# Optimization experiments

Measured on AMD Instinct MI355X. Metric: run time of the kernel, lower is better.

## Reference

```python
import jax, jax.numpy as jnp
import numpy as np

E = 16      # num_experts
K = 4       # num_experts_per_tok
H = 2048    # hidden_size
I = 1408    # moe_intermediate_size
SI = 5632   # shared expert intermediate size
CAP = 1024
NORM_TOPK = False


def setup_inputs() -> dict:
    key = jax.random.key(0)
    ks = jax.random.split(key, 9)
    def w(k, shape, fan_in):
        return jax.random.normal(k, shape, jnp.float32) * (fan_in ** -0.5)
    return {
        "hidden_states": jax.random.normal(ks[0], (1, 2048, H), jnp.float32),
        "gate_w":  w(ks[1], (E, H), H),        # router: Linear(H -> E), no bias
        "we_gate": w(ks[2], (E, I, H), H),     # per-expert gate_proj weights
        "we_up":   w(ks[3], (E, I, H), H),     # per-expert up_proj weights
        "we_down": w(ks[4], (E, H, I), I),     # per-expert down_proj weights
        "ws_gate": w(ks[5], (SI, H), H),       # shared expert gate_proj
        "ws_up":   w(ks[6], (SI, H), H),       # shared expert up_proj
        "ws_down": w(ks[7], (H, SI), SI),      # shared expert down_proj
        "sg_w":    w(ks[8], (1, H), H),        # shared_expert_gate: Linear(H -> 1)
    }


def reference(hidden_states, gate_w, we_gate, we_up, we_down,
              ws_gate, ws_up, ws_down, sg_w):
    B, S, Hd = hidden_states.shape
    x = hidden_states.reshape(-1, Hd)                      # [T, H]
    T = x.shape[0]

    # --- router ---
    router_logits = x @ gate_w.T                           # [T, E]
    probs = jax.nn.softmax(router_logits.astype(jnp.float32), axis=-1)
    topw, topi = jax.lax.top_k(probs, K)                   # [T, K]
    if NORM_TOPK:
        topw = topw / topw.sum(axis=-1, keepdims=True)

    # --- dispatch: flatten (token, slot) assignments ---
    A = T * K
    fe = topi.reshape(A)                                   # expert id per assignment
    fw = topw.reshape(A)                                   # routing weight per assignment
    ft = jnp.repeat(jnp.arange(T), K)                      # token id per assignment
    # position of each assignment within its expert (rank in arrival order)
    oh = jax.nn.one_hot(fe, E, dtype=jnp.int32)            # [A, E]
    pos = jnp.take_along_axis(jnp.cumsum(oh, axis=0) - 1, fe[:, None], axis=1)[:, 0]
    valid = pos < CAP
    # scatter tokens into per-expert buffers; overflow goes to dummy row CAP
    buf = jnp.zeros((E, CAP + 1, Hd), x.dtype)
    buf = buf.at[fe, jnp.where(valid, pos, CAP)].set(x[ft])[:, :CAP]  # [E, C, H]

    # --- per-expert SiLU-gated MLP (batched grouped GEMMs) ---
    g = jnp.einsum('ech,eih->eci', buf, we_gate)
    u = jnp.einsum('ech,eih->eci', buf, we_up)
    eo = jnp.einsum('eci,ehi->ech', jax.nn.silu(g) * u, we_down)      # [E, C, H]

    # --- combine: weighted scatter-add back to tokens ---
    ga = eo[fe, jnp.minimum(pos, CAP - 1)]                 # [A, H]
    wcomb = (fw * valid.astype(fw.dtype)).astype(x.dtype)
    y = jnp.zeros((T, Hd), x.dtype).at[ft].add(ga * wcomb[:, None])

    # --- shared expert with sigmoid gate ---
    sh = (jax.nn.silu(x @ ws_gate.T) * (x @ ws_up.T)) @ ws_down.T
    sh = jax.nn.sigmoid(x @ sg_w.T) * sh

    out = (y + sh).reshape(B, S, Hd)
    return out, router_logits
```

## Files before the change

### kernel.cpp

```cpp
#include <hip/hip_runtime.h>

#define T_TOK 2048
#define NE 16
#define KTOP 4
#define HD 2048
#define ID 1408
#define SID 5632
#define CAPACITY 1024

typedef __attribute__((ext_vector_type(8))) short short8;
typedef __attribute__((ext_vector_type(4))) float floatx4;

__device__ __forceinline__ short f2b(float f){
  union { float f; unsigned u; } v; v.f = f;
  unsigned r = v.u + 0x7fffu + ((v.u >> 16) & 1u);
  return (short)(r >> 16);
}
__device__ __forceinline__ float b2f(short s){
  union { float f; unsigned u; } v; v.u = ((unsigned)(unsigned short)s) << 16;
  return v.f;
}
__device__ __forceinline__ unsigned cvt_pk(float a, float b){
  unsigned r;
  asm("v_cvt_pk_bf16_f32 %0, %1, %2" : "=v"(r) : "v"(a), "v"(b));
  return r;
}
__device__ __forceinline__ short8 cvt8(float4 a, float4 b){
  union { unsigned d[4]; short8 s; } u;
  u.d[0] = cvt_pk(a.x, a.y); u.d[1] = cvt_pk(a.z, a.w);
  u.d[2] = cvt_pk(b.x, b.y); u.d[3] = cvt_pk(b.z, b.w);
  return u.s;
}
__device__ __forceinline__ void gl16(const void* g, void* l){
  __builtin_amdgcn_global_load_lds(
      (const __attribute__((address_space(1))) void*)g,
      (__attribute__((address_space(3))) void*)l, 16, 0, 0);
}

__global__ void moe_zero(int* __restrict__ counts){
  if (threadIdx.x < NE) counts[threadIdx.x] = 0;
}

__global__ void moe_convert(const float* __restrict__ eg, const float* __restrict__ eu,
                            const float* __restrict__ ed, const float* __restrict__ sgp,
                            const float* __restrict__ sup, const float* __restrict__ sdp,
                            short* __restrict__ dst)
{
  const long long R8 = 1441792LL;
  const int r = blockIdx.y;
  const float* src;
  if      (r <  4) src = eg  + (long long)r       * R8 * 8;
  else if (r <  8) src = eu  + (long long)(r - 4) * R8 * 8;
  else if (r < 12) src = ed  + (long long)(r - 8) * R8 * 8;
  else if (r == 12) src = sgp;
  else if (r == 13) src = sup;
  else              src = sdp;
  short8* d = (short8*)dst + (long long)r * R8;
  const long long stride = (long long)gridDim.x * blockDim.x;
  for (long long i = (long long)blockIdx.x * blockDim.x + threadIdx.x; i < R8; i += stride){
    float4 f0 = ((const float4*)src)[i * 2];
    float4 f1 = ((const float4*)src)[i * 2 + 1];
    d[i] = cvt8(f0, f1);
  }
}

__global__ void moe_router(const float* __restrict__ x,
                           const float* __restrict__ gate_w,
                           const float* __restrict__ sg_w,
                           float* __restrict__ logits_out,
                           short* __restrict__ xb,
                           int* __restrict__ counts,
                           int* __restrict__ slot_token,
                           float* __restrict__ slot_w,
                           int* __restrict__ tslot,
                           float* __restrict__ tw,
                           float* __restrict__ sg)
{
  int wave = threadIdx.x >> 6, lane = threadIdx.x & 63;
  int t = (blockIdx.x << 2) + wave;
  if (t >= T_TOK) return;
  const float4* xr = (const float4*)(x + (size_t)t * HD);
  short8* xbw = (short8*)(xb + (size_t)t * HD);
  float acc[17];
  #pragma unroll
  for (int e = 0; e < 17; ++e) acc[e] = 0.f;
  #pragma unroll
  for (int j = 0; j < 4; ++j){
    int i4 = (j * 64 + lane) * 2;
    float4 x0 = xr[i4], x1 = xr[i4 + 1];
    xbw[j * 64 + lane] = cvt8(x0, x1);
    #pragma unroll
    for (int e = 0; e < 16; ++e){
      const float4* gr = (const float4*)(gate_w + e * HD);
      float4 g0 = gr[i4], g1 = gr[i4 + 1];
      acc[e] += x0.x*g0.x + x0.y*g0.y + x0.z*g0.z + x0.w*g0.w
              + x1.x*g1.x + x1.y*g1.y + x1.z*g1.z + x1.w*g1.w;
    }
    const float4* sr = (const float4*)sg_w;
    float4 s0 = sr[i4], s1 = sr[i4 + 1];
    acc[16] += x0.x*s0.x + x0.y*s0.y + x0.z*s0.z + x0.w*s0.w
             + x1.x*s1.x + x1.y*s1.y + x1.z*s1.z + x1.w*s1.w;
  }
  #pragma unroll
  for (int e = 0; e < 17; ++e){
    float v = acc[e];
    #pragma unroll
    for (int off = 32; off > 0; off >>= 1) v += __shfl_xor(v, off, 64);
    acc[e] = v;
  }
  if (lane == 0){
    float m = acc[0];
    #pragma unroll
    for (int e = 1; e < 16; ++e) m = fmaxf(m, acc[e]);
    float p[16]; float s = 0.f;
    #pragma unroll
    for (int e = 0; e < 16; ++e){ p[e] = expf(acc[e] - m); s += p[e]; }
    float inv = 1.f / s;
    #pragma unroll
    for (int e = 0; e < 16; ++e) logits_out[t * 16 + e] = acc[e];
    unsigned used = 0;
    for (int k = 0; k < KTOP; ++k){
      float best = -1.f; int bi = 0;
      #pragma unroll
      for (int e = 0; e < 16; ++e){
        float pe = ((used >> e) & 1u) ? -1.f : p[e];
        if (pe > best){ best = pe; bi = e; }
      }
      used |= (1u << bi);
      int pos = atomicAdd(&counts[bi], 1);
      int enc = -1;
      if (pos < CAPACITY){
        slot_token[bi * CAPACITY + pos] = t;
        slot_w[bi * CAPACITY + pos] = best * inv;
        enc = bi * CAPACITY + pos;
      }
      tslot[t * KTOP + k] = enc;
      tw[t * KTOP + k] = best * inv;
    }
    sg[t] = 1.f / (1.f + expf(-acc[16]));
  }
}


#define GEMM_PREAMBLE \
  const int tid = threadIdx.x; \
  const int lane = tid & 63, wave = tid >> 6; \
  const int wr = wave >> 1, wc = wave & 1; \
  const int lrow = lane & 15, lk = lane >> 4; \
  const int s_th = (tid & 7) ^ ((tid >> 3) & 7); \
  const int koff = (s_th & 3) << 3; \
  const int rloc = ((tid >> 3) << 1) + (s_th >> 2); \
  const int lb = lrow >> 1; \
  const int soff = (((((lrow & 1) << 2) | lk) ^ (lb & 7)) << 4); \
  const int abase = (wr * 32 + lb) * 128 + soff;

__global__ __launch_bounds__(256) void moe_gateup(
    const short* __restrict__ Asrc,
    const short* __restrict__ Wg, const short* __restrict__ Wu,
    short* __restrict__ Out,
    const int* __restrict__ counts, const int* __restrict__ slot_token,
    int Ndim, int Kdim, int expert_mode, int mtiles, int ntiles)
{
  int nwg = gridDim.x;
  int wg = ((blockIdx.x & 7) * (nwg >> 3)) + (blockIdx.x >> 3);
  int m_t = wg % mtiles; wg /= mtiles;
  int n_t = wg % ntiles; int e = wg / ntiles;

  int cnt = T_TOK; size_t woff = 0; short* out = Out;
  if (expert_mode){
    cnt = counts[e]; if (cnt > CAPACITY) cnt = CAPACITY;
    if (m_t * 128 >= cnt) return;
    woff = (size_t)e * Ndim * Kdim;
    out = Out + (size_t)e * CAPACITY * Ndim;
  }
  const int m0 = m_t * 128, n0 = n_t * 64;

  __shared__ __align__(16) char smem[2][16384];

  GEMM_PREAMBLE
  const int gbase = 8192 + (wc * 16 + lb) * 128 + soff;

  const short* aP[2];
  #pragma unroll
  for (int i = 0; i < 2; ++i){
    int p = m0 + i * 64 + rloc;
    const short* base;
    if (expert_mode){
      int q = (p < cnt) ? p : 0;
      base = Asrc + (size_t)slot_token[e * CAPACITY + q] * Kdim;
    } else base = Asrc + (size_t)p * Kdim;
    aP[i] = base + koff;
  }
  const short* bgP = Wg + woff + (size_t)(n0 + rloc) * Kdim + koff;
  const short* buP = Wu + woff + (size_t)(n0 + rloc) * Kdim + koff;

  const floatx4 vzero = {0.f, 0.f, 0.f, 0.f};
  floatx4 accg[4][2], accu[4][2];
  #pragma unroll
  for (int i = 0; i < 4; ++i)
    #pragma unroll
    for (int j = 0; j < 2; ++j){ accg[i][j] = vzero; accu[i][j] = vzero; }

#define GU_STAGE(B, K) { char* _b = smem[B]; \
    gl16(aP[0] + (K), _b + tid * 16); \
    gl16(aP[1] + (K), _b + 4096 + tid * 16); \
    gl16(bgP + (K),   _b + 8192 + tid * 16); \
    gl16(buP + (K),   _b + 12288 + tid * 16); }

#define GU_COMPUTE(B) { const char* bb = smem[B]; \
    short8 a[4], bg[2], bu[2]; \
    _Pragma("unroll") \
    for (int mf = 0; mf < 4; ++mf) a[mf] = *(const short8*)(bb + abase + mf * 1024); \
    _Pragma("unroll") \
    for (int nf = 0; nf < 2; ++nf){ \
      bg[nf] = *(const short8*)(bb + gbase + nf * 1024); \
      bu[nf] = *(const short8*)(bb + gbase + 4096 + nf * 1024); } \
    _Pragma("unroll") \
    for (int mf = 0; mf < 4; ++mf) \
      _Pragma("unroll") \
      for (int nf = 0; nf < 2; ++nf){ \
        accg[mf][nf] = __builtin_amdgcn_mfma_f32_16x16x32_bf16(a[mf], bg[nf], accg[mf][nf], 0, 0, 0); \
        accu[mf][nf] = __builtin_amdgcn_mfma_f32_16x16x32_bf16(a[mf], bu[nf], accu[mf][nf], 0, 0, 0); } }

  const int NSTEP = Kdim >> 5;
  GU_STAGE(0, 0)
  int cur = 0;
  for (int s = 0; s < NSTEP - 1; ++s){
    GU_STAGE(cur ^ 1, (s + 1) << 5)
    asm volatile("s_waitcnt vmcnt(4)" ::: "memory");
    asm volatile("s_barrier" ::: "memory");
    GU_COMPUTE(cur)
    asm volatile("s_barrier" ::: "memory");
    cur ^= 1;
  }
  asm volatile("s_waitcnt vmcnt(0)" ::: "memory");
  asm volatile("s_barrier" ::: "memory");
  GU_COMPUTE(cur)

  const int colbase = n0 + wc * 32 + lrow;
  #pragma unroll
  for (int mf = 0; mf < 4; ++mf){
    int pr = m0 + wr * 64 + mf * 16 + lk * 4;
    #pragma unroll
    for (int nf = 0; nf < 2; ++nf){
      floatx4 g4 = accg[mf][nf], u4 = accu[mf][nf];
      int col = colbase + nf * 16;
      #pragma unroll
      for (int r = 0; r < 4; ++r){
        float gv = g4[r], uv = u4[r];
        float a = (gv / (1.f + __expf(-gv))) * uv;
        out[(size_t)(pr + r) * Ndim + col] = f2b(a);
      }
    }
  }
}

template<int NF>
__global__ __launch_bounds__(256) void moe_down(
    const short* __restrict__ Asrc, const short* __restrict__ Wd,
    float* __restrict__ y, short* __restrict__ eo,
    const int* __restrict__ counts, const int* __restrict__ slot_token,
    const float* __restrict__ slot_w, const float* __restrict__ sgate,
    int Kdim, int expert_mode, int mtiles, int ntiles)
{
  int nwg = gridDim.x;
  int wg = ((blockIdx.x & 7) * (nwg >> 3)) + (blockIdx.x >> 3);
  int m_t = wg % mtiles; wg /= mtiles;
  int n_t = wg % ntiles; int e = wg / ntiles;

  int cnt = T_TOK; const short* ab = Asrc; size_t woff = 0;
  if (expert_mode){
    cnt = counts[e]; if (cnt > CAPACITY) cnt = CAPACITY;
    if (m_t * 128 >= cnt) return;
    ab = Asrc + (size_t)e * CAPACITY * Kdim;
    woff = (size_t)e * HD * Kdim;
  }
  const int m0 = m_t * 128, n0 = n_t * (NF * 32);

  __shared__ __align__(16) char smem[2][8192 + NF * 2048];

  GEMM_PREAMBLE
  const int bbase = 8192 + (wc * (NF * 8) + lb) * 128 + soff;

  const short* aP[2];
  #pragma unroll
  for (int i = 0; i < 2; ++i)
    aP[i] = ab + (size_t)(m0 + i * 64 + rloc) * Kdim + koff;
  const short* bP[NF / 2];
  #pragma unroll
  for (int i = 0; i < NF / 2; ++i)
    bP[i] = Wd + woff + (size_t)(n0 + i * 64 + rloc) * Kdim + koff;

  const floatx4 vzero = {0.f, 0.f, 0.f, 0.f};
  floatx4 acc[4][NF];
  #pragma unroll
  for (int i = 0; i < 4; ++i)
    #pragma unroll
    for (int j = 0; j < NF; ++j) acc[i][j] = vzero;

#define DN_STAGE(B, K) { char* _b = smem[B]; \
    gl16(aP[0] + (K), _b + tid * 16); \
    gl16(aP[1] + (K), _b + 4096 + tid * 16); \
    _Pragma("unroll") \
    for (int i = 0; i < NF / 2; ++i) \
      gl16(bP[i] + (K), _b + 8192 + i * 4096 + tid * 16); }

#define DN_COMPUTE(B) { const char* bb = smem[B]; \
    short8 a[4], b[NF]; \
    _Pragma("unroll") \
    for (int mf = 0; mf < 4; ++mf) a[mf] = *(const short8*)(bb + abase + mf * 1024); \
    _Pragma("unroll") \
    for (int nf = 0; nf < NF; ++nf) b[nf] = *(const short8*)(bb + bbase + nf * 1024); \
    _Pragma("unroll") \
    for (int mf = 0; mf < 4; ++mf) \
      _Pragma("unroll") \
      for (int nf = 0; nf < NF; ++nf) \
        acc[mf][nf] = __builtin_amdgcn_mfma_f32_16x16x32_bf16(a[mf], b[nf], acc[mf][nf], 0, 0, 0); }

  const int NSTEP = Kdim >> 5;
  DN_STAGE(0, 0)
  int cur = 0;
  for (int s = 0; s < NSTEP - 1; ++s){
    DN_STAGE(cur ^ 1, (s + 1) << 5)
    if (NF == 4) asm volatile("s_waitcnt vmcnt(4)" ::: "memory");
    else         asm volatile("s_waitcnt vmcnt(3)" ::: "memory");
    asm volatile("s_barrier" ::: "memory");
    DN_COMPUTE(cur)
    asm volatile("s_barrier" ::: "memory");
    cur ^= 1;
  }
  asm volatile("s_waitcnt vmcnt(0)" ::: "memory");
  asm volatile("s_barrier" ::: "memory");
  DN_COMPUTE(cur)

  const int colb = n0 + wc * (NF * 16) + lrow;
  if (expert_mode){
    if (eo){
      #pragma unroll
      for (int mf = 0; mf < 4; ++mf){
        int pr = m0 + wr * 64 + mf * 16 + lk * 4;
        #pragma unroll
        for (int r = 0; r < 4; ++r){
          int p = pr + r;
          #pragma unroll
          for (int nf = 0; nf < NF; ++nf)
            eo[(size_t)(e * CAPACITY + p) * HD + colb + nf * 16] = f2b(acc[mf][nf][r]);
        }
      }
    } else {
      #pragma unroll
      for (int mf = 0; mf < 4; ++mf){
        int pr = m0 + wr * 64 + mf * 16 + lk * 4;
        #pragma unroll
        for (int r = 0; r < 4; ++r){
          int p = pr + r;
          if (p < cnt){
            int tok = slot_token[e * CAPACITY + p];
            float w = slot_w[e * CAPACITY + p];
            #pragma unroll
            for (int nf = 0; nf < NF; ++nf)
              atomicAdd(&y[(size_t)tok * HD + colb + nf * 16], w * acc[mf][nf][r]);
          }
        }
      }
    }
  } else {
    #pragma unroll
    for (int mf = 0; mf < 4; ++mf){
      int pr = m0 + wr * 64 + mf * 16 + lk * 4;
      #pragma unroll
      for (int r = 0; r < 4; ++r){
        int t = pr + r;
        float sv = sgate[t];
        #pragma unroll
        for (int nf = 0; nf < NF; ++nf)
          y[(size_t)t * HD + colb + nf * 16] = sv * acc[mf][nf][r];
      }
    }
  }
}

__global__ void moe_combine(const short* __restrict__ eo,
                            const int* __restrict__ tslot,
                            const float* __restrict__ tw,
                            float* __restrict__ y)
{
  int t = blockIdx.x;
  int o = threadIdx.x << 3;
  float* yp = y + (size_t)t * HD + o;
  float4 a0 = *(const float4*)yp, a1 = *(const float4*)(yp + 4);
  float acc[8] = {a0.x, a0.y, a0.z, a0.w, a1.x, a1.y, a1.z, a1.w};
  #pragma unroll
  for (int k = 0; k < KTOP; ++k){
    int s = tslot[t * KTOP + k];
    if (s >= 0){
      float w = tw[t * KTOP + k];
      short8 v = *(const short8*)(eo + (size_t)s * HD + o);
      #pragma unroll
      for (int j = 0; j < 8; ++j) acc[j] += w * b2f(v[j]);
    }
  }
  float4 r0 = {acc[0], acc[1], acc[2], acc[3]};
  float4 r1 = {acc[4], acc[5], acc[6], acc[7]};
  *(float4*)yp = r0; *(float4*)(yp + 4) = r1;
}

extern "C" void kernel_launch(void* const* d_in, const int* in_sizes, int n_in,
                              void* d_out, int out_size, void* d_ws, size_t ws_size,
                              hipStream_t stream)
{
  (void)in_sizes; (void)n_in; (void)out_size; (void)ws_size;
  const float* x       = (const float*)d_in[0];
  const float* gate_w  = (const float*)d_in[1];
  const float* we_gate = (const float*)d_in[2];
  const float* we_up   = (const float*)d_in[3];
  const float* we_down = (const float*)d_in[4];
  const float* wsg     = (const float*)d_in[5];
  const float* wsu     = (const float*)d_in[6];
  const float* wsd     = (const float*)d_in[7];
  const float* sg_w    = (const float*)d_in[8];

  float* y      = (float*)d_out;
  float* logits = y + (size_t)T_TOK * HD;

  const size_t N_EW = (size_t)NE * ID * HD;
  const size_t N_SW = (size_t)SID * HD;

  char* ws = (char*)d_ws;
  size_t off = 0;
  short* xb   = (short*)(ws + off); off += (size_t)T_TOK * HD * 2;
  short* wb   = (short*)(ws + off); off += (3 * N_EW + 3 * N_SW) * 2;
  short* act  = (short*)(ws + off); off += (size_t)NE * CAPACITY * ID * 2;
  short* acts = (short*)(ws + off); off += (size_t)T_TOK * SID * 2;
  int*   slot_token = (int*)  (ws + off); off += 65536;
  float* slot_w     = (float*)(ws + off); off += 65536;
  int*   tslot      = (int*)  (ws + off); off += 32768;
  float* tw         = (float*)(ws + off); off += 32768;
  int*   counts     = (int*)  (ws + off); off += 256;
  float* sg         = (float*)(ws + off);

  short* wbeg = wb;
  short* wbeu = wb + N_EW;
  short* wbed = wb + 2 * N_EW;
  short* wbsg = wb + 3 * N_EW;
  short* wbsu = wb + 3 * N_EW + N_SW;
  short* wbsd = wb + 3 * N_EW + 2 * N_SW;
  short* eo = wbeg;

  moe_zero<<<1, 64, 0, stream>>>(counts);
  moe_convert<<<dim3(256, 15), 256, 0, stream>>>(we_gate, we_up, we_down,
                                                 wsg, wsu, wsd, wb);
  moe_router<<<512, 256, 0, stream>>>(x, gate_w, sg_w, logits, xb,
                                      counts, slot_token, slot_w, tslot, tw, sg);
  moe_gateup<<<16 * 88, 256, 0, stream>>>(xb, wbsg, wbsu, acts,
                                          nullptr, nullptr, SID, HD, 0, 16, 88);
  moe_gateup<<<8 * 22 * NE, 256, 0, stream>>>(xb, wbeg, wbeu, act,
                                              counts, slot_token, ID, HD, 1, 8, 22);
  moe_down<2><<<16 * 32, 256, 0, stream>>>(acts, wbsd, y, nullptr, nullptr, nullptr,
                                           nullptr, sg, SID, 0, 16, 32);
  moe_down<4><<<8 * 16 * NE, 256, 0, stream>>>(act, wbed, y, eo, counts, slot_token,
                                               slot_w, nullptr, ID, 1, 8, 16);
  moe_combine<<<T_TOK, 256, 0, stream>>>(eo, tslot, tw, y);
}
```

Measured before the change: 860.7 us.

## Fuse weight bf16 conversion into router and GEMM launches to overlap work

Removes the standalone weight-conversion kernel and splits its work into extra workgroups appended to the router and the two gate/up GEMM launches. Each launch converts the weights needed by a later stage while doing its own compute, so the memory-bound conversion can overlap with compute-bound GEMMs. The atomic-add path in the down kernel, now unused, is also removed. The extra conversion blocks compete for bandwidth and compute units with the GEMM tiles, and correctness depends on launch order, since each stage must only read weights converted by an earlier launch.

```diff
diff --git a/kernel.cpp b/kernel.cpp
--- a/kernel.cpp
+++ b/kernel.cpp
@@ -37,31 +37,26 @@
       (__attribute__((address_space(3))) void*)l, 16, 0, 0);
 }
 
+__device__ __forceinline__ void conv_range(
+    int cb, int ncb,
+    const float* __restrict__ s1, short* __restrict__ d1, long long n1,
+    const float* __restrict__ s2, short* __restrict__ d2, long long n2)
+{
+  const long long tot = n1 + n2;
+  const long long stride = (long long)ncb * 256;
+  #pragma unroll 2
+  for (long long i = (long long)cb * 256 + threadIdx.x; i < tot; i += stride){
+    const float* s; short8* d; long long j;
+    if (i < n1){ s = s1; d = (short8*)d1; j = i; }
+    else       { s = s2; d = (short8*)d2; j = i - n1; }
+    float4 f0 = ((const float4*)s)[j * 2];
+    float4 f1 = ((const float4*)s)[j * 2 + 1];
+    d[j] = cvt8(f0, f1);
+  }
+}
+
 __global__ void moe_zero(int* __restrict__ counts){
   if (threadIdx.x < NE) counts[threadIdx.x] = 0;
-}
-
-__global__ void moe_convert(const float* __restrict__ eg, const float* __restrict__ eu,
-                            const float* __restrict__ ed, const float* __restrict__ sgp,
-                            const float* __restrict__ sup, const float* __restrict__ sdp,
-                            short* __restrict__ dst)
-{
-  const long long R8 = 1441792LL;
-  const int r = blockIdx.y;
-  const float* src;
-  if      (r <  4) src = eg  + (long long)r       * R8 * 8;
-  else if (r <  8) src = eu  + (long long)(r - 4) * R8 * 8;
-  else if (r < 12) src = ed  + (long long)(r - 8) * R8 * 8;
-  else if (r == 12) src = sgp;
-  else if (r == 13) src = sup;
-  else              src = sdp;
-  short8* d = (short8*)dst + (long long)r * R8;
-  const long long stride = (long long)gridDim.x * blockDim.x;
-  for (long long i = (long long)blockIdx.x * blockDim.x + threadIdx.x; i < R8; i += stride){
-    float4 f0 = ((const float4*)src)[i * 2];
-    float4 f1 = ((const float4*)src)[i * 2 + 1];
-    d[i] = cvt8(f0, f1);
-  }
 }
 
 __global__ void moe_router(const float* __restrict__ x,
@@ -74,11 +69,16 @@
                            float* __restrict__ slot_w,
                            int* __restrict__ tslot,
                            float* __restrict__ tw,
-                           float* __restrict__ sg)
-{
+                           float* __restrict__ sg,
+                           const float* cs1, short* cd1, long long cn1,
+                           const float* cs2, short* cd2, long long cn2)
+{
+  if (blockIdx.x >= 512){
+    conv_range(blockIdx.x - 512, gridDim.x - 512, cs1, cd1, cn1, cs2, cd2, cn2);
+    return;
+  }
   int wave = threadIdx.x >> 6, lane = threadIdx.x & 63;
   int t = (blockIdx.x << 2) + wave;
-  if (t >= T_TOK) return;
   const float4* xr = (const float4*)(x + (size_t)t * HD);
   short8* xbw = (short8*)(xb + (size_t)t * HD);
   float acc[17];
@@ -159,10 +159,17 @@
     const short* __restrict__ Wg, const short* __restrict__ Wu,
     short* __restrict__ Out,
     const int* __restrict__ counts, const int* __restrict__ slot_token,
-    int Ndim, int Kdim, int expert_mode, int mtiles, int ntiles)
-{
-  int nwg = gridDim.x;
-  int wg = ((blockIdx.x & 7) * (nwg >> 3)) + (blockIdx.x >> 3);
+    int Ndim, int Kdim, int expert_mode, int mtiles, int ntiles,
+    const float* cs1, short* cd1, long long cn1,
+    const float* cs2, short* cd2, long long cn2, int conv_nwg)
+{
+  if ((int)blockIdx.x < conv_nwg){
+    conv_range(blockIdx.x, conv_nwg, cs1, cd1, cn1, cs2, cd2, cn2);
+    return;
+  }
+  int nwg = gridDim.x - conv_nwg;
+  int bid = blockIdx.x - conv_nwg;
+  int wg = ((bid & 7) * (nwg >> 3)) + (bid >> 3);
   int m_t = wg % mtiles; wg /= mtiles;
   int n_t = wg % ntiles; int e = wg / ntiles;
 
@@ -335,33 +342,15 @@
 
   const int colb = n0 + wc * (NF * 16) + lrow;
   if (expert_mode){
-    if (eo){
+    #pragma unroll
+    for (int mf = 0; mf < 4; ++mf){
+      int pr = m0 + wr * 64 + mf * 16 + lk * 4;
       #pragma unroll
-      for (int mf = 0; mf < 4; ++mf){
-        int pr = m0 + wr * 64 + mf * 16 + lk * 4;
+      for (int r = 0; r < 4; ++r){
+        int p = pr + r;
         #pragma unroll
-        for (int r = 0; r < 4; ++r){
-          int p = pr + r;
-          #pragma unroll
-          for (int nf = 0; nf < NF; ++nf)
-            eo[(size_t)(e * CAPACITY + p) * HD + colb + nf * 16] = f2b(acc[mf][nf][r]);
-        }
-      }
-    } else {
-      #pragma unroll
-      for (int mf = 0; mf < 4; ++mf){
-        int pr = m0 + wr * 64 + mf * 16 + lk * 4;
-        #pragma unroll
-        for (int r = 0; r < 4; ++r){
-          int p = pr + r;
-          if (p < cnt){
-            int tok = slot_token[e * CAPACITY + p];
-            float w = slot_w[e * CAPACITY + p];
-            #pragma unroll
-            for (int nf = 0; nf < NF; ++nf)
-              atomicAdd(&y[(size_t)tok * HD + colb + nf * 16], w * acc[mf][nf][r]);
-          }
-        }
+        for (int nf = 0; nf < NF; ++nf)
+          eo[(size_t)(e * CAPACITY + p) * HD + colb + nf * 16] = f2b(acc[mf][nf][r]);
       }
     }
   } else {
@@ -425,6 +414,8 @@
 
   const size_t N_EW = (size_t)NE * ID * HD;
   const size_t N_SW = (size_t)SID * HD;
+  const long long G_EW = (long long)(N_EW / 8);
+  const long long G_SW = (long long)(N_SW / 8);
 
   char* ws = (char*)d_ws;
   size_t off = 0;
@@ -448,14 +439,15 @@
   short* eo = wbeg;
 
   moe_zero<<<1, 64, 0, stream>>>(counts);
-  moe_convert<<<dim3(256, 15), 256, 0, stream>>>(we_gate, we_up, we_down,
-                                                 wsg, wsu, wsd, wb);
-  moe_router<<<512, 256, 0, stream>>>(x, gate_w, sg_w, logits, xb,
-                                      counts, slot_token, slot_w, tslot, tw, sg);
-  moe_gateup<<<16 * 88, 256, 0, stream>>>(xb, wbsg, wbsu, acts,
-                                          nullptr, nullptr, SID, HD, 0, 16, 88);
-  moe_gateup<<<8 * 22 * NE, 256, 0, stream>>>(xb, wbeg, wbeu, act,
-                                              counts, slot_token, ID, HD, 1, 8, 22);
+  moe_router<<<512 + 512, 256, 0, stream>>>(x, gate_w, sg_w, logits, xb,
+                                            counts, slot_token, slot_w, tslot, tw, sg,
+                                            wsg, wbsg, G_SW, wsu, wbsu, G_SW);
+  moe_gateup<<<512 + 16 * 88, 256, 0, stream>>>(xb, wbsg, wbsu, acts,
+                                                nullptr, nullptr, SID, HD, 0, 16, 88,
+                                                we_gate, wbeg, G_EW, we_up, wbeu, G_EW, 512);
+  moe_gateup<<<512 + 8 * 22 * NE, 256, 0, stream>>>(xb, wbeg, wbeu, act,
+                                                    counts, slot_token, ID, HD, 1, 8, 22,
+                                                    we_down, wbed, G_EW, wsd, wbsd, G_SW, 512);
   moe_down<2><<<16 * 32, 256, 0, stream>>>(acts, wbsd, y, nullptr, nullptr, nullptr,
                                            nullptr, sg, SID, 0, 16, 32);
   moe_down<4><<<8 * 16 * NE, 256, 0, stream>>>(act, wbed, y, eo, counts, slot_token,
```

Result: faster. 797.4 us (-7.3%).
